# Kernel tuning notes

Measured on AMD Instinct MI355X. Metric: run time of the kernel, lower is better.

The kernel has to match this reference:

```python
import jax, jax.numpy as jnp
import numpy as np


def setup_inputs() -> dict:
    key = jax.random.key(0)
    k1, k2 = jax.random.split(key)
    B, H, W = 32, 1024, 1024
    x = jax.random.normal(k1, (B, 2, H, W), dtype=jnp.float32)
    gt = jax.random.randint(k2, (B, H, W), 0, 2, dtype=jnp.int32)
    return {"x": x, "gt": gt}


def _bbox_stats(mask, H, W):
    # mask: [B,H,W] bool. Reproduces torch.where(mask)->min/max of row (dim0)
    # and col (dim1) indices per sample, fully vectorized.
    rows = jnp.any(mask, axis=2)  # [B,H] rows containing a positive
    cols = jnp.any(mask, axis=1)  # [B,W] cols containing a positive
    r = jnp.arange(H, dtype=jnp.int32)[None, :]
    c = jnp.arange(W, dtype=jnp.int32)[None, :]
    rmin = jnp.min(jnp.where(rows, r, H), axis=1).astype(jnp.float32)
    rmax = jnp.max(jnp.where(rows, r, -1), axis=1).astype(jnp.float32)
    cmin = jnp.min(jnp.where(cols, c, W), axis=1).astype(jnp.float32)
    cmax = jnp.max(jnp.where(cols, c, -1), axis=1).astype(jnp.float32)
    # NOTE: original divides row coords by w and col coords by h (kept faithful)
    center_x = (rmin + rmax) / 2.0 / W
    center_y = (cmin + cmax) / 2.0 / H
    length = jnp.square((rmax - rmin) / W) + jnp.square((cmax - cmin) / H)
    return center_x, center_y, length


def reference(x, gt):
    B, _, H, W = x.shape
    # CrossEntropyLoss over 2 classes, mean over B*H*W
    logp = jax.nn.log_softmax(x, axis=1)  # [B,2,H,W]
    picked = jnp.take_along_axis(logp, gt[:, None, :, :].astype(jnp.int32), axis=1)[:, 0]
    cel_loss = -jnp.mean(picked)

    area = jnp.float32(W * H * B)
    trans_x = x[:, 1, :, :] > x[:, 0, :, :]  # [B,H,W] bool (non-differentiable, as in torch)
    area_loss = jnp.square(jnp.sum(trans_x).astype(jnp.float32) / area
                           - jnp.sum(gt).astype(jnp.float32) / area)

    # dist terms only if every sample has nonempty gt and prediction masks
    flag = jnp.all((jnp.sum(gt, axis=(1, 2)) > 0)
                   & (jnp.sum(trans_x, axis=(1, 2)) > 0)).astype(jnp.float32)

    xcx, xcy, xlen = _bbox_stats(trans_x, H, W)
    gcx, gcy, glen = _bbox_stats(gt == 1, H, W)
    dist_c = jnp.mean(jnp.square(xcx - gcx) + jnp.square(xcy - gcy))
    dist_length = jnp.mean(jnp.square(xlen - glen))

    return cel_loss + area_loss + 0.5 * flag * (dist_c + dist_length)
```

## Files before the change

### kernel.cpp

```cpp
#include <hip/hip_runtime.h>
#include <math.h>

#define HH 1024
#define WW 1024
#define BB 32
#define HW (HH*WW)
#define CHUNKS 64
#define PIXB (HW/CHUNKS)
#define THREADS 256
#define ITERS (PIXB/4/THREADS)
#define NBLK (BB*CHUNKS)

typedef float f32x4 __attribute__((ext_vector_type(4)));
typedef int   i32x4 __attribute__((ext_vector_type(4)));

struct WsLayout {
    float cel_part[NBLK];
    int tcnt[NBLK], gcnt[NBLK];
    int trmin[NBLK], trmax[NBLK], tcmin[NBLK], tcmax[NBLK];
    int grmin[NBLK], grmax[NBLK], gcmin[NBLK], gcmax[NBLK];
};

__global__ __launch_bounds__(THREADS) void wnet_main(
        const float* __restrict__ x, const int* __restrict__ gt,
        WsLayout* __restrict__ ws) {
    const int blk   = blockIdx.x;
    const int b     = blk >> 6;
    const int chunk = blk & 63;
    const f32x4* __restrict__ x0 = reinterpret_cast<const f32x4*>(x + (size_t)b * 2 * HW);
    const f32x4* __restrict__ x1 = reinterpret_cast<const f32x4*>(x + (size_t)b * 2 * HW + HW);
    const i32x4* __restrict__ g  = reinterpret_cast<const i32x4*>(gt + (size_t)b * HW);
    const int base4    = chunk * (PIXB/4);
    const int wavebase = threadIdx.x & ~63;

    float cel = 0.0f;
    int tc = 0, gc = 0;
    int trmin = HH, trmax = -1, tcmin = WW, tcmax = -1;
    int grmin = HH, grmax = -1, gcmin = WW, gcmax = -1;

    #pragma unroll 4
    for (int it = 0; it < ITERS; ++it) {
        const int idx4 = base4 + it*THREADS + threadIdx.x;
        const f32x4 a  = __builtin_nontemporal_load(&x0[idx4]);
        const f32x4 c  = __builtin_nontemporal_load(&x1[idx4]);
        const i32x4 gv = __builtin_nontemporal_load(&g[idx4]);
        const int p0 = (base4 + it*THREADS + wavebase) << 2;
        const int h  = p0 >> 10;
        const int wb = p0 & 1023;

        #pragma unroll
        for (int j = 0; j < 4; ++j) {
            const float xa = a[j];
            const float xc = c[j];
            const bool t = xc > xa;
            const bool m = (gv[j] == 1);
            const unsigned long long bt = __ballot(t);
            const unsigned long long bg = __ballot(m);
            tc += __popcll(bt);
            gc += __popcll(bg);
            if (bt) {
                trmin = min(trmin, h);  trmax = max(trmax, h);
                tcmin = min(tcmin, wb + (__builtin_ctzll(bt) << 2) + j);
                tcmax = max(tcmax, wb + ((63 - __builtin_clzll(bt)) << 2) + j);
            }
            if (bg) {
                grmin = min(grmin, h);  grmax = max(grmax, h);
                gcmin = min(gcmin, wb + (__builtin_ctzll(bg) << 2) + j);
                gcmax = max(gcmax, wb + ((63 - __builtin_clzll(bg)) << 2) + j);
            }
            const float d = m ? (xa - xc) : (xc - xa);
            cel += fmaxf(d, 0.0f) + __logf(1.0f + __expf(-fabsf(d)));
        }
    }

    #pragma unroll
    for (int o = 32; o > 0; o >>= 1) cel += __shfl_down(cel, o);

    __shared__ float s_cel[4];
    __shared__ int   s_v[4][10];
    const int wid  = threadIdx.x >> 6;
    const int lane = threadIdx.x & 63;
    if (lane == 0) {
        s_cel[wid]  = cel;
        s_v[wid][0] = tc;    s_v[wid][1] = gc;
        s_v[wid][2] = trmin; s_v[wid][3] = trmax;
        s_v[wid][4] = tcmin; s_v[wid][5] = tcmax;
        s_v[wid][6] = grmin; s_v[wid][7] = grmax;
        s_v[wid][8] = gcmin; s_v[wid][9] = gcmax;
    }
    __syncthreads();
    if (threadIdx.x == 0) {
        ws->cel_part[blk] = s_cel[0] + s_cel[1] + s_cel[2] + s_cel[3];
        ws->tcnt[blk]  = s_v[0][0] + s_v[1][0] + s_v[2][0] + s_v[3][0];
        ws->gcnt[blk]  = s_v[0][1] + s_v[1][1] + s_v[2][1] + s_v[3][1];
        ws->trmin[blk] = min(min(s_v[0][2], s_v[1][2]), min(s_v[2][2], s_v[3][2]));
        ws->trmax[blk] = max(max(s_v[0][3], s_v[1][3]), max(s_v[2][3], s_v[3][3]));
        ws->tcmin[blk] = min(min(s_v[0][4], s_v[1][4]), min(s_v[2][4], s_v[3][4]));
        ws->tcmax[blk] = max(max(s_v[0][5], s_v[1][5]), max(s_v[2][5], s_v[3][5]));
        ws->grmin[blk] = min(min(s_v[0][6], s_v[1][6]), min(s_v[2][6], s_v[3][6]));
        ws->grmax[blk] = max(max(s_v[0][7], s_v[1][7]), max(s_v[2][7], s_v[3][7]));
        ws->gcmin[blk] = min(min(s_v[0][8], s_v[1][8]), min(s_v[2][8], s_v[3][8]));
        ws->gcmax[blk] = max(max(s_v[0][9], s_v[1][9]), max(s_v[2][9], s_v[3][9]));
    }
}

__device__ __forceinline__ float sqf(float v) { return v * v; }

__global__ __launch_bounds__(256) void wnet_finalize(
        const WsLayout* __restrict__ ws, float* __restrict__ out) {
    __shared__ float s_cel[4];
    __shared__ float s_dc[BB], s_dl[BB];
    __shared__ int   s_tc[BB], s_gc[BB], s_fl[BB];

    float c = 0.0f;
    for (int i = threadIdx.x; i < NBLK; i += 256) c += ws->cel_part[i];
    #pragma unroll
    for (int o = 32; o > 0; o >>= 1) c += __shfl_down(c, o);
    const int wid  = threadIdx.x >> 6;
    const int lane = threadIdx.x & 63;
    if (lane == 0) s_cel[wid] = c;

    const int b    = threadIdx.x >> 3;
    const int part = threadIdx.x & 7;
    int tcs = 0, gcs = 0;
    int a1 = HH, a2 = -1, a3 = WW, a4 = -1;
    int a5 = HH, a6 = -1, a7 = WW, a8 = -1;
    #pragma unroll
    for (int k = 0; k < 8; ++k) {
        const int idx = b*64 + part*8 + k;
        tcs += ws->tcnt[idx];  gcs += ws->gcnt[idx];
        a1 = min(a1, ws->trmin[idx]);  a2 = max(a2, ws->trmax[idx]);
        a3 = min(a3, ws->tcmin[idx]);  a4 = max(a4, ws->tcmax[idx]);
        a5 = min(a5, ws->grmin[idx]);  a6 = max(a6, ws->grmax[idx]);
        a7 = min(a7, ws->gcmin[idx]);  a8 = max(a8, ws->gcmax[idx]);
    }
    #pragma unroll
    for (int o = 4; o > 0; o >>= 1) {
        tcs += __shfl_down(tcs, o, 8);  gcs += __shfl_down(gcs, o, 8);
        a1 = min(a1, __shfl_down(a1, o, 8));  a2 = max(a2, __shfl_down(a2, o, 8));
        a3 = min(a3, __shfl_down(a3, o, 8));  a4 = max(a4, __shfl_down(a4, o, 8));
        a5 = min(a5, __shfl_down(a5, o, 8));  a6 = max(a6, __shfl_down(a6, o, 8));
        a7 = min(a7, __shfl_down(a7, o, 8));  a8 = max(a8, __shfl_down(a8, o, 8));
    }
    if (part == 0) {
        const float xrmin = (float)a1, xrmax = (float)a2;
        const float xcmin = (float)a3, xcmax = (float)a4;
        const float yrmin = (float)a5, yrmax = (float)a6;
        const float ycmin = (float)a7, ycmax = (float)a8;
        const float xcx  = (xrmin + xrmax) * 0.5f / (float)WW;
        const float xcy  = (xcmin + xcmax) * 0.5f / (float)HH;
        const float xlen = sqf((xrmax - xrmin) / (float)WW) + sqf((xcmax - xcmin) / (float)HH);
        const float gcx  = (yrmin + yrmax) * 0.5f / (float)WW;
        const float gcy  = (ycmin + ycmax) * 0.5f / (float)HH;
        const float glen = sqf((yrmax - yrmin) / (float)WW) + sqf((ycmax - ycmin) / (float)HH);
        s_dc[b] = sqf(xcx - gcx) + sqf(xcy - gcy);
        s_dl[b] = sqf(xlen - glen);
        s_tc[b] = tcs;  s_gc[b] = gcs;
        s_fl[b] = (tcs > 0 && gcs > 0) ? 1 : 0;
    }
    __syncthreads();
    if (threadIdx.x == 0) {
        const float celT = s_cel[0] + s_cel[1] + s_cel[2] + s_cel[3];
        int tcT = 0, gcT = 0, fl = 1;
        float dc = 0.0f, dl = 0.0f;
        for (int i = 0; i < BB; ++i) {
            tcT += s_tc[i];  gcT += s_gc[i];
            fl  &= s_fl[i];
            dc  += s_dc[i];  dl += s_dl[i];
        }
        const float area = (float)HW * (float)BB;
        const float cel_loss = celT / area;
        const float al = ((float)tcT - (float)gcT) / area;
        const float area_loss = al * al;
        const float dist_c = dc / (float)BB;
        const float dist_l = dl / (float)BB;
        out[0] = cel_loss + area_loss + 0.5f * (float)fl * (dist_c + dist_l);
    }
}

extern "C" void kernel_launch(void* const* d_in, const int* in_sizes, int n_in,
                              void* d_out, int out_size, void* d_ws, size_t ws_size,
                              hipStream_t stream) {
    const float* x  = (const float*)d_in[0];
    const int*   gt = (const int*)d_in[1];
    float* out = (float*)d_out;
    WsLayout* ws = (WsLayout*)d_ws;

    hipLaunchKernelGGL(wnet_main, dim3(NBLK), dim3(THREADS), 0, stream, x, gt, ws);
    hipLaunchKernelGGL(wnet_finalize, dim3(1), dim3(256), 0, stream, ws, out);
}
```

Before: 77.28 us.

## Replace per-element wave ballots with per-thread bitmasks reduced after the loop

Tracks row occupancy as a per-iteration bitmask and column occupancy as a per-thread OR of lane masks, then resolves bounding boxes with a single round of ballots and shuffles after the streaming loop. Counts are packed into one 32-bit value and reduced alongside the loss sum. The cross-entropy term is rewritten without a select on the sign of the difference. This removes ballot and branch work from the hot loop of a kernel that is largely bandwidth-bound.

```diff
diff --git a/kernel.cpp b/kernel.cpp
--- a/kernel.cpp
+++ b/kernel.cpp
@@ -21,6 +21,8 @@
     int grmin[NBLK], grmax[NBLK], gcmin[NBLK], gcmax[NBLK];
 };
 
+__device__ __forceinline__ float sqf(float v) { return v * v; }
+
 __global__ __launch_bounds__(THREADS) void wnet_main(
         const float* __restrict__ x, const int* __restrict__ gt,
         WsLayout* __restrict__ ws) {
@@ -28,15 +30,15 @@
     const int b     = blk >> 6;
     const int chunk = blk & 63;
     const f32x4* __restrict__ x0 = reinterpret_cast<const f32x4*>(x + (size_t)b * 2 * HW);
-    const f32x4* __restrict__ x1 = reinterpret_cast<const f32x4*>(x + (size_t)b * 2 * HW + HW);
+    const f32x4* __restrict__ x1 = x0 + (HW/4);
     const i32x4* __restrict__ g  = reinterpret_cast<const i32x4*>(gt + (size_t)b * HW);
-    const int base4    = chunk * (PIXB/4);
-    const int wavebase = threadIdx.x & ~63;
+    const int base4 = chunk * (PIXB/4);
+    const int row0  = chunk * 16;
 
     float cel = 0.0f;
-    int tc = 0, gc = 0;
-    int trmin = HH, trmax = -1, tcmin = WW, tcmax = -1;
-    int grmin = HH, grmax = -1, gcmin = WW, gcmax = -1;
+    int cnt_t = 0, cnt_g = 0;
+    unsigned int umask_t = 0u, umask_g = 0u;
+    unsigned int rmask_t = 0u, rmask_g = 0u;
 
     #pragma unroll 4
     for (int it = 0; it < ITERS; ++it) {
@@ -44,37 +46,52 @@
         const f32x4 a  = __builtin_nontemporal_load(&x0[idx4]);
         const f32x4 c  = __builtin_nontemporal_load(&x1[idx4]);
         const i32x4 gv = __builtin_nontemporal_load(&g[idx4]);
-        const int p0 = (base4 + it*THREADS + wavebase) << 2;
-        const int h  = p0 >> 10;
-        const int wb = p0 & 1023;
-
+        unsigned int it_t = 0u, it_g = 0u;
         #pragma unroll
         for (int j = 0; j < 4; ++j) {
             const float xa = a[j];
             const float xc = c[j];
-            const bool t = xc > xa;
-            const bool m = (gv[j] == 1);
-            const unsigned long long bt = __ballot(t);
-            const unsigned long long bg = __ballot(m);
-            tc += __popcll(bt);
-            gc += __popcll(bg);
-            if (bt) {
-                trmin = min(trmin, h);  trmax = max(trmax, h);
-                tcmin = min(tcmin, wb + (__builtin_ctzll(bt) << 2) + j);
-                tcmax = max(tcmax, wb + ((63 - __builtin_clzll(bt)) << 2) + j);
-            }
-            if (bg) {
-                grmin = min(grmin, h);  grmax = max(grmax, h);
-                gcmin = min(gcmin, wb + (__builtin_ctzll(bg) << 2) + j);
-                gcmax = max(gcmax, wb + ((63 - __builtin_clzll(bg)) << 2) + j);
-            }
-            const float d = m ? (xa - xc) : (xc - xa);
-            cel += fmaxf(d, 0.0f) + __logf(1.0f + __expf(-fabsf(d)));
-        }
-    }
-
-    #pragma unroll
-    for (int o = 32; o > 0; o >>= 1) cel += __shfl_down(cel, o);
+            it_t |= (xc > xa)    ? (1u << j) : 0u;
+            it_g |= (gv[j] == 1) ? (1u << j) : 0u;
+            const float s = xc - xa;
+            cel += fmaxf(s, 0.0f) - ((gv[j] == 1) ? s : 0.0f)
+                 + __logf(1.0f + __expf(-fabsf(s)));
+        }
+        cnt_t += __builtin_popcount(it_t);
+        cnt_g += __builtin_popcount(it_g);
+        umask_t |= it_t;  umask_g |= it_g;
+        rmask_t |= (it_t ? 1u : 0u) << it;
+        rmask_g |= (it_g ? 1u : 0u) << it;
+    }
+
+    unsigned int cnts = (unsigned int)cnt_t | ((unsigned int)cnt_g << 16);
+    unsigned int rmsk = rmask_t | (rmask_g << 16);
+    #pragma unroll
+    for (int o = 32; o > 0; o >>= 1) {
+        cel  += __shfl_down(cel, o);
+        cnts += __shfl_down(cnts, o);
+        rmsk |= __shfl_down(rmsk, o);
+    }
+    const unsigned int rT = rmsk & 0xFFFFu, rG = rmsk >> 16;
+    int rmin_t = HH, rmax_t = -1, rmin_g = HH, rmax_g = -1;
+    if (rT) { rmin_t = row0 + __builtin_ctz(rT); rmax_t = row0 + 31 - __builtin_clz(rT); }
+    if (rG) { rmin_g = row0 + __builtin_ctz(rG); rmax_g = row0 + 31 - __builtin_clz(rG); }
+
+    const int wcb = (threadIdx.x & ~63) << 2;
+    int cmin_t = WW, cmax_t = -1, cmin_g = WW, cmax_g = -1;
+    #pragma unroll
+    for (int j = 0; j < 4; ++j) {
+        const unsigned long long bt = __ballot((umask_t >> j) & 1u);
+        const unsigned long long bg = __ballot((umask_g >> j) & 1u);
+        if (bt) {
+            cmin_t = min(cmin_t, wcb + (__builtin_ctzll(bt) << 2) + j);
+            cmax_t = max(cmax_t, wcb + ((63 - __builtin_clzll(bt)) << 2) + j);
+        }
+        if (bg) {
+            cmin_g = min(cmin_g, wcb + (__builtin_ctzll(bg) << 2) + j);
+            cmax_g = max(cmax_g, wcb + ((63 - __builtin_clzll(bg)) << 2) + j);
+        }
+    }
 
     __shared__ float s_cel[4];
     __shared__ int   s_v[4][10];
@@ -82,11 +99,11 @@
     const int lane = threadIdx.x & 63;
     if (lane == 0) {
         s_cel[wid]  = cel;
-        s_v[wid][0] = tc;    s_v[wid][1] = gc;
-        s_v[wid][2] = trmin; s_v[wid][3] = trmax;
-        s_v[wid][4] = tcmin; s_v[wid][5] = tcmax;
-        s_v[wid][6] = grmin; s_v[wid][7] = grmax;
-        s_v[wid][8] = gcmin; s_v[wid][9] = gcmax;
+        s_v[wid][0] = (int)(cnts & 0xFFFFu);  s_v[wid][1] = (int)(cnts >> 16);
+        s_v[wid][2] = rmin_t; s_v[wid][3] = rmax_t;
+        s_v[wid][4] = cmin_t; s_v[wid][5] = cmax_t;
+        s_v[wid][6] = rmin_g; s_v[wid][7] = rmax_g;
+        s_v[wid][8] = cmin_g; s_v[wid][9] = cmax_g;
     }
     __syncthreads();
     if (threadIdx.x == 0) {
@@ -103,8 +120,6 @@
         ws->gcmax[blk] = max(max(s_v[0][9], s_v[1][9]), max(s_v[2][9], s_v[3][9]));
     }
 }
-
-__device__ __forceinline__ float sqf(float v) { return v * v; }
 
 __global__ __launch_bounds__(256) void wnet_finalize(
         const WsLayout* __restrict__ ws, float* __restrict__ out) {
@@ -171,10 +186,8 @@
         const float area = (float)HW * (float)BB;
         const float cel_loss = celT / area;
         const float al = ((float)tcT - (float)gcT) / area;
-        const float area_loss = al * al;
-        const float dist_c = dc / (float)BB;
-        const float dist_l = dl / (float)BB;
-        out[0] = cel_loss + area_loss + 0.5f * (float)fl * (dist_c + dist_l);
+        out[0] = cel_loss + al * al
+               + 0.5f * (float)fl * (dc / (float)BB + dl / (float)BB);
     }
 }
 
```

Measured after the change: 73.61 us. 1.05x faster.
